# Performance work log

Hardware: AMD Instinct MI355X
Metric: run time of the kernel (lower is better)

## Reference

```python
import jax, jax.numpy as jnp
import numpy as np

E = 1024  # embed_dim
H = 16    # num_heads
D = E // H  # head_dim


def setup_inputs() -> dict:
    key = jax.random.key(0)
    ks = jax.random.split(key, 9)
    s = 0.02
    return {
        "hidden_state": jax.random.normal(ks[0], (4, 1024, E), jnp.float32),
        "Wq": jax.random.normal(ks[1], (H, D, E), jnp.float32) * s,
        "bq": jax.random.normal(ks[2], (H, D), jnp.float32) * s,
        "Wk": jax.random.normal(ks[3], (H, D, E), jnp.float32) * s,
        "bk": jax.random.normal(ks[4], (H, D), jnp.float32) * s,
        "Wv": jax.random.normal(ks[5], (H, D, E), jnp.float32) * s,
        "bv": jax.random.normal(ks[6], (H, D), jnp.float32) * s,
        "Wo": jax.random.normal(ks[7], (E, E), jnp.float32) * s,
        "bo": jax.random.normal(ks[8], (E,), jnp.float32) * s,
    }


def _mha(x, Wq, bq, Wk, bk, Wv, bv, Wo, bo):
    # Per-head linear projections (torch Linear: y = x W^T + b), batched over heads.
    q = jnp.einsum("bse,hde->bhsd", x, Wq) + bq[None, :, None, :]
    k = jnp.einsum("bse,hde->bhsd", x, Wk) + bk[None, :, None, :]
    v = jnp.einsum("bse,hde->bhsd", x, Wv) + bv[None, :, None, :]
    scores = jnp.einsum("bhsd,bhtd->bhst", q, k) / jnp.sqrt(jnp.asarray(D, x.dtype))
    w = jax.nn.softmax(scores, axis=-1)  # F.softmax default -> last dim
    o = jnp.einsum("bhst,bhtd->bhsd", w, v)
    # concat heads along last dim: [B,S,H*D] in head order (matches torch.cat)
    B, _, S, _ = o.shape
    o = jnp.transpose(o, (0, 2, 1, 3)).reshape(B, S, H * D)
    return o @ Wo.T + bo


def reference(hidden_state, Wq, bq, Wk, bk, Wv, bv, Wo, bo):
    return _mha(hidden_state, Wq, bq, Wk, bk, Wv, bv, Wo, bo)
```

## Files before the change

kernel.cpp:

```cpp
#include <hip/hip_runtime.h>
#include <hip/hip_bf16.h>
#include <stdint.h>

#define E_DIM 1024
#define H_NUM 16
#define D_DIM 64
#define B_NUM 4
#define S_LEN 1024

typedef __attribute__((ext_vector_type(8))) short bf16x8;
typedef __attribute__((ext_vector_type(4))) short bf16x4;
typedef __attribute__((ext_vector_type(4))) float f32x4;

__device__ inline ushort f2b(float x) {
    __hip_bfloat16 h = __float2bfloat16(x);
    return *(ushort*)&h;
}
__device__ inline uint pk2(float a, float b) {
    __hip_bfloat162 h = __float22bfloat162_rn(make_float2(a, b));
    return *(uint*)&h;
}

__device__ inline void gld16(const ushort* g, ushort* l) {
    __builtin_amdgcn_global_load_lds((const __attribute__((address_space(1))) void*)g,
                                     (__attribute__((address_space(3))) void*)l, 16, 0, 0);
}

__global__ __launch_bounds__(256)
void convert_all(const float* __restrict__ X,  const float* __restrict__ Wq,
                 const float* __restrict__ Wk, const float* __restrict__ Wv,
                 const float* __restrict__ Wo,
                 ushort* __restrict__ Xb, ushort* __restrict__ Wcat,
                 ushort* __restrict__ Wob)
{
    const int bid = blockIdx.x;
    const float* src; ushort* dst; size_t off;
    if (bid < 4096)      { src = X;  dst = Xb;   off = (size_t)bid * 1024; }
    else if (bid < 5120) { src = Wq; dst = Wcat;              off = (size_t)(bid - 4096) * 1024; }
    else if (bid < 6144) { src = Wk; dst = Wcat + (1u << 20); off = (size_t)(bid - 5120) * 1024; }
    else if (bid < 7168) { src = Wv; dst = Wcat + (2u << 20); off = (size_t)(bid - 6144) * 1024; }
    else                 { src = Wo; dst = Wob;               off = (size_t)(bid - 7168) * 1024; }
    const size_t i = off + (size_t)threadIdx.x * 4;
    float4 v = *(const float4*)&src[i];
    ushort4 o;
    o.x = f2b(v.x); o.y = f2b(v.y); o.z = f2b(v.z); o.w = f2b(v.w);
    *(ushort4*)&dst[i] = o;
}

template<int MODE>
__global__ __launch_bounds__(256)
void gemm128(const ushort* __restrict__ A, const ushort* __restrict__ Bw,
             const float* __restrict__ b0, const float* __restrict__ b1,
             const float* __restrict__ b2,
             ushort* __restrict__ Qb, ushort* __restrict__ Kb,
             ushort* __restrict__ Vt_g, float* __restrict__ Cout, int K)
{
    constexpr int BM = 128;
    constexpr int BN = (MODE == 0) ? 128 : 64;
    constexpr int MI = (MODE == 0) ? 4 : 2;
    constexpr int NI = 4;

    __shared__ ushort As[2][BM * 32];
    __shared__ ushort Bs[2][BN * 32];

    const int tid  = threadIdx.x;
    const int wave = tid >> 6;
    const int lane = tid & 63;
    const int quad = lane >> 4;
    const int l16  = lane & 15;
    const int wm   = (MODE == 0) ? (wave & 1) : wave;
    const int wn   = (MODE == 0) ? (wave >> 1) : 0;
    const int moff = wm * MI * 16;
    const int noff = wn * NI * 16;
    const int m0   = blockIdx.x * BM;
    const int n0   = blockIdx.y * BN;

    f32x4 acc[MI][NI] = {};

#pragma unroll
    for (int i = 0; i < BM / 64; ++i) {
        const int e = i * 256 + tid;
        gld16(&A[(size_t)(m0 + (e >> 2)) * K + (e & 3) * 8], &As[0][e * 8]);
    }
#pragma unroll
    for (int i = 0; i < BN / 64; ++i) {
        const int e = i * 256 + tid;
        gld16(&Bw[(size_t)(n0 + (e >> 2)) * K + (e & 3) * 8], &Bs[0][e * 8]);
    }
    __syncthreads();

    const int nk = K >> 5;
    for (int ki = 0; ki < nk; ++ki) {
        const int cur = ki & 1;
        if (ki + 1 < nk) {
            const int k0 = (ki + 1) << 5;
#pragma unroll
            for (int i = 0; i < BM / 64; ++i) {
                const int e = i * 256 + tid;
                gld16(&A[(size_t)(m0 + (e >> 2)) * K + k0 + (e & 3) * 8], &As[cur ^ 1][e * 8]);
            }
#pragma unroll
            for (int i = 0; i < BN / 64; ++i) {
                const int e = i * 256 + tid;
                gld16(&Bw[(size_t)(n0 + (e >> 2)) * K + k0 + (e & 3) * 8], &Bs[cur ^ 1][e * 8]);
            }
        }

        bf16x8 af[MI], bf[NI];
#pragma unroll
        for (int mi = 0; mi < MI; ++mi)
            af[mi] = *(const bf16x8*)&As[cur][(moff + mi * 16 + l16) * 32 + quad * 8];
#pragma unroll
        for (int ni = 0; ni < NI; ++ni)
            bf[ni] = *(const bf16x8*)&Bs[cur][(noff + ni * 16 + l16) * 32 + quad * 8];
#pragma unroll
        for (int mi = 0; mi < MI; ++mi)
#pragma unroll
            for (int ni = 0; ni < NI; ++ni)
                acc[mi][ni] = __builtin_amdgcn_mfma_f32_16x16x32_bf16(af[mi], bf[ni], acc[mi][ni], 0, 0, 0);
        __syncthreads();
    }

    if (MODE == 0) {
        const int seg = n0 >> 10;
        const float* bp = (seg == 0) ? b0 : (seg == 1) ? b1 : b2;
        if (seg < 2) {
            ushort* dst = (seg == 0) ? Qb : Kb;
#pragma unroll
            for (int ni = 0; ni < NI; ++ni) {
                const int c = (n0 + noff + ni * 16 + l16) & 1023;
                const float bv = bp[c];
#pragma unroll
                for (int mi = 0; mi < MI; ++mi)
#pragma unroll
                    for (int r = 0; r < 4; ++r) {
                        const int m = m0 + moff + mi * 16 + quad * 4 + r;
                        dst[(size_t)m * 1024 + c] = f2b(acc[mi][ni][r] + bv);
                    }
            }
        } else {
#pragma unroll
            for (int ni = 0; ni < NI; ++ni) {
                const int c  = (n0 + noff + ni * 16 + l16) & 1023;
                const int hh = c >> 6, d = c & 63;
                const float bv = bp[c];
#pragma unroll
                for (int mi = 0; mi < MI; ++mi) {
                    const int mb = m0 + moff + mi * 16 + quad * 4;
                    const int b  = mb >> 10, s = mb & 1023;
                    ushort4 pk;
                    pk.x = f2b(acc[mi][ni][0] + bv);
                    pk.y = f2b(acc[mi][ni][1] + bv);
                    pk.z = f2b(acc[mi][ni][2] + bv);
                    pk.w = f2b(acc[mi][ni][3] + bv);
                    *(ushort4*)&Vt_g[(((size_t)(b * 16 + hh)) * 64 + d) * 1024 + s] = pk;
                }
            }
        }
    } else {
#pragma unroll
        for (int ni = 0; ni < NI; ++ni) {
            const int n = n0 + noff + ni * 16 + l16;
            const float bv = b0[n];
#pragma unroll
            for (int mi = 0; mi < MI; ++mi)
#pragma unroll
                for (int r = 0; r < 4; ++r) {
                    const int m = m0 + moff + mi * 16 + quad * 4 + r;
                    Cout[(size_t)m * 1024 + n] = acc[mi][ni][r] + bv;
                }
        }
    }
}

__global__ __launch_bounds__(256)
void attention4(const ushort* __restrict__ Qg, const ushort* __restrict__ Kg,
                const ushort* __restrict__ Vg, ushort* __restrict__ Og)
{
    __shared__ ushort S[4][64][68];

    const int tid  = threadIdx.x;
    const int w    = tid >> 6;
    const int lane = tid & 63;
    const int quad = lane >> 4;
    const int l16  = lane & 15;

    const int qt = blockIdx.x;
    const int bh = blockIdx.y;
    const int b  = bh >> 4;
    const int h  = bh & 15;
    const size_t tbase = ((size_t)b * S_LEN) * E_DIM + (size_t)h * D_DIM;
    const size_t vbase = (size_t)bh * D_DIM * S_LEN;

    const int sr = tid >> 3;
    const int c8 = (tid & 7) * 8;

#pragma unroll
    for (int g = 0; g < 2; ++g) {
        const int rr = sr + g * 32;
        *(uint4*)&S[2][rr][c8] = *(const uint4*)&Qg[tbase + (size_t)(qt * 64 + rr) * E_DIM + c8];
        *(uint4*)&S[0][rr][c8] = *(const uint4*)&Kg[tbase + (size_t)rr * E_DIM + c8];
        *(uint4*)&S[1][rr][c8] = *(const uint4*)&Vg[vbase + (size_t)rr * S_LEN + c8];
    }
    __syncthreads();

    bf16x8 qf[2];
    qf[0] = *(const bf16x8*)&S[2][w * 16 + l16][quad * 8];
    qf[1] = *(const bf16x8*)&S[2][w * 16 + l16][32 + quad * 8];
    __syncthreads();

    float lq = 0.0f;
    f32x4 oacc[4] = {};
    const float C2 = 0.18033688011f;

    for (int kt = 0; kt < 16; ++kt) {
        const int cur = kt & 1;

        uint4 kpre[2], vpre[2];
        if (kt < 15) {
#pragma unroll
            for (int g = 0; g < 2; ++g) {
                const int rr = sr + g * 32;
                kpre[g] = *(const uint4*)&Kg[tbase + (size_t)((kt + 1) * 64 + rr) * E_DIM + c8];
                vpre[g] = *(const uint4*)&Vg[vbase + (size_t)rr * S_LEN + (kt + 1) * 64 + c8];
            }
        }

        f32x4 sacc[4] = {};
#pragma unroll
        for (int mt = 0; mt < 4; ++mt)
#pragma unroll
            for (int ks = 0; ks < 2; ++ks) {
                bf16x8 kf = *(const bf16x8*)&S[cur * 2][mt * 16 + l16][ks * 32 + quad * 8];
                sacc[mt] = __builtin_amdgcn_mfma_f32_16x16x32_bf16(kf, qf[ks], sacc[mt], 0, 0, 0);
            }

        float p[4][4], rs = 0.0f;
#pragma unroll
        for (int mt = 0; mt < 4; ++mt)
#pragma unroll
            for (int r = 0; r < 4; ++r) {
                p[mt][r] = exp2f(sacc[mt][r] * C2);
                rs += p[mt][r];
            }
        lq += rs;

        bf16x4 pf[4];
#pragma unroll
        for (int kb = 0; kb < 4; ++kb) {
            union { uint u[2]; bf16x4 v; } pk;
            pk.u[0] = pk2(p[kb][0], p[kb][1]);
            pk.u[1] = pk2(p[kb][2], p[kb][3]);
            pf[kb] = pk.v;
        }

#pragma unroll
        for (int nb = 0; nb < 4; ++nb)
#pragma unroll
            for (int kb = 0; kb < 4; ++kb) {
                bf16x4 vf = *(const bf16x4*)&S[cur * 2 + 1][nb * 16 + l16][kb * 16 + quad * 4];
                oacc[nb] = __builtin_amdgcn_mfma_f32_16x16x16bf16_1k(pf[kb], vf, oacc[nb], 0, 0, 0);
            }

        if (kt < 15) {
            const int nxt = cur ^ 1;
#pragma unroll
            for (int g = 0; g < 2; ++g) {
                const int rr = sr + g * 32;
                *(uint4*)&S[nxt * 2][rr][c8]     = kpre[g];
                *(uint4*)&S[nxt * 2 + 1][rr][c8] = vpre[g];
            }
        }
        __syncthreads();
    }

    lq += __shfl_xor(lq, 16);
    lq += __shfl_xor(lq, 32);
    const float linv = 1.0f / lq;
    float lC[4];
#pragma unroll
    for (int r = 0; r < 4; ++r) lC[r] = __shfl(linv, quad * 4 + r);
#pragma unroll
    for (int nb = 0; nb < 4; ++nb)
#pragma unroll
        for (int r = 0; r < 4; ++r) {
            const int q = qt * 64 + w * 16 + quad * 4 + r;
            const int d = nb * 16 + l16;
            Og[tbase + (size_t)q * E_DIM + d] = f2b(oacc[nb][r] * lC[r]);
        }
}

extern "C" void kernel_launch(void* const* d_in, const int* in_sizes, int n_in,
                              void* d_out, int out_size, void* d_ws, size_t ws_size,
                              hipStream_t stream)
{
    (void)in_sizes; (void)n_in; (void)out_size; (void)ws_size;

    const float* X  = (const float*)d_in[0];
    const float* Wq = (const float*)d_in[1];
    const float* bq = (const float*)d_in[2];
    const float* Wk = (const float*)d_in[3];
    const float* bk = (const float*)d_in[4];
    const float* Wv = (const float*)d_in[5];
    const float* bv = (const float*)d_in[6];
    const float* Wo = (const float*)d_in[7];
    const float* bo = (const float*)d_in[8];

    const size_t MEG = 1u << 20;
    ushort* ws   = (ushort*)d_ws;
    ushort* Xb   = ws;
    ushort* Wcat = ws + 4 * MEG;
    ushort* Wob  = ws + 7 * MEG;
    ushort* Qb   = ws + 8 * MEG;
    ushort* Kb   = ws + 12 * MEG;
    ushort* Vtg  = ws + 16 * MEG;
    ushort* AO   = Xb;

    dim3 blk(256);

    convert_all<<<8192, blk, 0, stream>>>(X, Wq, Wk, Wv, Wo, Xb, Wcat, Wob);

    gemm128<0><<<dim3(32, 24), blk, 0, stream>>>(Xb, Wcat, bq, bk, bv,
                                                 Qb, Kb, Vtg, nullptr, E_DIM);

    attention4<<<dim3(16, 64), blk, 0, stream>>>(Qb, Kb, Vtg, AO);

    gemm128<1><<<dim3(32, 16), blk, 0, stream>>>(AO, Wob, bo, nullptr, nullptr,
                                                 nullptr, nullptr, nullptr,
                                                 (float*)d_out, E_DIM);
}
```

Before: 203.0 us.

## Retile GEMMs, stage epilogues through LDS, fold softmax scale into Q, double attention rows

The QKV projection GEMM now uses 128x64 tiles, which doubles the grid. Its epilogue stages results through shared memory so that the row-major Q/K and the transposed V can be written with wide coalesced 16-byte stores; the output GEMM stages fp32 results the same way. The softmax scale (log2e/sqrt(D)) is folded into Q at projection time, so the attention kernel no longer multiplies scores before exp2. Each attention block now handles 128 query rows and reuses every K/V tile across two query groups, which halves K/V reloads at the cost of more registers and half as many blocks.

```diff
diff --git a/kernel.cpp b/kernel.cpp
--- a/kernel.cpp
+++ b/kernel.cpp
@@ -11,6 +11,8 @@
 typedef __attribute__((ext_vector_type(8))) short bf16x8;
 typedef __attribute__((ext_vector_type(4))) short bf16x4;
 typedef __attribute__((ext_vector_type(4))) float f32x4;
+
+#define SOFTMAX_C2 0.18033688011112042f
 
 __device__ inline ushort f2b(float x) {
     __hip_bfloat16 h = __float2bfloat16(x);
@@ -55,38 +57,28 @@
              ushort* __restrict__ Qb, ushort* __restrict__ Kb,
              ushort* __restrict__ Vt_g, float* __restrict__ Cout, int K)
 {
-    constexpr int BM = 128;
-    constexpr int BN = (MODE == 0) ? 128 : 64;
-    constexpr int MI = (MODE == 0) ? 4 : 2;
-    constexpr int NI = 4;
-
-    __shared__ ushort As[2][BM * 32];
-    __shared__ ushort Bs[2][BN * 32];
+    __shared__ __align__(16) ushort SM[12288];
+    ushort* As = SM;
+    ushort* Bs = SM + 8192;
 
     const int tid  = threadIdx.x;
     const int wave = tid >> 6;
     const int lane = tid & 63;
     const int quad = lane >> 4;
     const int l16  = lane & 15;
-    const int wm   = (MODE == 0) ? (wave & 1) : wave;
-    const int wn   = (MODE == 0) ? (wave >> 1) : 0;
-    const int moff = wm * MI * 16;
-    const int noff = wn * NI * 16;
-    const int m0   = blockIdx.x * BM;
-    const int n0   = blockIdx.y * BN;
-
-    f32x4 acc[MI][NI] = {};
-
-#pragma unroll
-    for (int i = 0; i < BM / 64; ++i) {
+    const int wm   = wave & 1;
+    const int wn   = wave >> 1;
+    const int m0   = blockIdx.x * 128;
+    const int n0   = blockIdx.y * 64;
+
+    f32x4 acc[4][2] = {};
+
+#pragma unroll
+    for (int i = 0; i < 2; ++i) {
         const int e = i * 256 + tid;
-        gld16(&A[(size_t)(m0 + (e >> 2)) * K + (e & 3) * 8], &As[0][e * 8]);
-    }
-#pragma unroll
-    for (int i = 0; i < BN / 64; ++i) {
-        const int e = i * 256 + tid;
-        gld16(&Bw[(size_t)(n0 + (e >> 2)) * K + (e & 3) * 8], &Bs[0][e * 8]);
-    }
+        gld16(&A[(size_t)(m0 + (e >> 2)) * K + (e & 3) * 8], &As[e * 8]);
+    }
+    gld16(&Bw[(size_t)(n0 + (tid >> 2)) * K + (tid & 3) * 8], &Bs[tid * 8]);
     __syncthreads();
 
     const int nk = K >> 5;
@@ -95,86 +87,117 @@
         if (ki + 1 < nk) {
             const int k0 = (ki + 1) << 5;
 #pragma unroll
-            for (int i = 0; i < BM / 64; ++i) {
+            for (int i = 0; i < 2; ++i) {
                 const int e = i * 256 + tid;
-                gld16(&A[(size_t)(m0 + (e >> 2)) * K + k0 + (e & 3) * 8], &As[cur ^ 1][e * 8]);
-            }
-#pragma unroll
-            for (int i = 0; i < BN / 64; ++i) {
-                const int e = i * 256 + tid;
-                gld16(&Bw[(size_t)(n0 + (e >> 2)) * K + k0 + (e & 3) * 8], &Bs[cur ^ 1][e * 8]);
-            }
-        }
-
-        bf16x8 af[MI], bf[NI];
-#pragma unroll
-        for (int mi = 0; mi < MI; ++mi)
-            af[mi] = *(const bf16x8*)&As[cur][(moff + mi * 16 + l16) * 32 + quad * 8];
-#pragma unroll
-        for (int ni = 0; ni < NI; ++ni)
-            bf[ni] = *(const bf16x8*)&Bs[cur][(noff + ni * 16 + l16) * 32 + quad * 8];
-#pragma unroll
-        for (int mi = 0; mi < MI; ++mi)
-#pragma unroll
-            for (int ni = 0; ni < NI; ++ni)
+                gld16(&A[(size_t)(m0 + (e >> 2)) * K + k0 + (e & 3) * 8],
+                      &As[(cur ^ 1) * 4096 + e * 8]);
+            }
+            gld16(&Bw[(size_t)(n0 + (tid >> 2)) * K + k0 + (tid & 3) * 8],
+                  &Bs[(cur ^ 1) * 2048 + tid * 8]);
+        }
+
+        bf16x8 af[4], bf[2];
+#pragma unroll
+        for (int mi = 0; mi < 4; ++mi)
+            af[mi] = *(const bf16x8*)&As[cur * 4096 + (wm * 64 + mi * 16 + l16) * 32 + quad * 8];
+#pragma unroll
+        for (int ni = 0; ni < 2; ++ni)
+            bf[ni] = *(const bf16x8*)&Bs[cur * 2048 + (wn * 32 + ni * 16 + l16) * 32 + quad * 8];
+#pragma unroll
+        for (int mi = 0; mi < 4; ++mi)
+#pragma unroll
+            for (int ni = 0; ni < 2; ++ni)
                 acc[mi][ni] = __builtin_amdgcn_mfma_f32_16x16x32_bf16(af[mi], bf[ni], acc[mi][ni], 0, 0, 0);
         __syncthreads();
     }
 
     if (MODE == 0) {
-        const int seg = n0 >> 10;
+        const int seg   = n0 >> 10;
+        const int cbase = n0 & 1023;
         const float* bp = (seg == 0) ? b0 : (seg == 1) ? b1 : b2;
+        const float scl = (seg == 0) ? SOFTMAX_C2 : 1.0f;
+
         if (seg < 2) {
+            ushort* T = SM;
+#pragma unroll
+            for (int ni = 0; ni < 2; ++ni) {
+                const int nloc = wn * 32 + ni * 16 + l16;
+                const float bv = bp[cbase + nloc];
+#pragma unroll
+                for (int mi = 0; mi < 4; ++mi)
+#pragma unroll
+                    for (int r = 0; r < 4; ++r)
+                        T[(wm * 64 + mi * 16 + quad * 4 + r) * 72 + nloc] =
+                            f2b((acc[mi][ni][r] + bv) * scl);
+            }
+            __syncthreads();
             ushort* dst = (seg == 0) ? Qb : Kb;
-#pragma unroll
-            for (int ni = 0; ni < NI; ++ni) {
-                const int c = (n0 + noff + ni * 16 + l16) & 1023;
-                const float bv = bp[c];
-#pragma unroll
-                for (int mi = 0; mi < MI; ++mi)
-#pragma unroll
-                    for (int r = 0; r < 4; ++r) {
-                        const int m = m0 + moff + mi * 16 + quad * 4 + r;
-                        dst[(size_t)m * 1024 + c] = f2b(acc[mi][ni][r] + bv);
-                    }
-            }
+            const int row = tid >> 1, half = tid & 1;
+            const ushort* s = &T[row * 72 + half * 32];
+            ushort* d = &dst[(size_t)(m0 + row) * 1024 + cbase + half * 32];
+#pragma unroll
+            for (int j = 0; j < 4; ++j)
+                *(uint4*)(d + j * 8) = *(const uint4*)(s + j * 8);
         } else {
-#pragma unroll
-            for (int ni = 0; ni < NI; ++ni) {
-                const int c  = (n0 + noff + ni * 16 + l16) & 1023;
-                const int hh = c >> 6, d = c & 63;
-                const float bv = bp[c];
-#pragma unroll
-                for (int mi = 0; mi < MI; ++mi) {
-                    const int mb = m0 + moff + mi * 16 + quad * 4;
-                    const int b  = mb >> 10, s = mb & 1023;
+            ushort* Tt = SM;
+            const int hh = cbase >> 6;
+            const int b  = m0 >> 10, sbase = m0 & 1023;
+#pragma unroll
+            for (int ni = 0; ni < 2; ++ni) {
+                const int nloc = wn * 32 + ni * 16 + l16;
+                const float bv = bp[cbase + nloc];
+#pragma unroll
+                for (int mi = 0; mi < 4; ++mi) {
+                    const int mloc = wm * 64 + mi * 16 + quad * 4;
                     ushort4 pk;
                     pk.x = f2b(acc[mi][ni][0] + bv);
                     pk.y = f2b(acc[mi][ni][1] + bv);
                     pk.z = f2b(acc[mi][ni][2] + bv);
                     pk.w = f2b(acc[mi][ni][3] + bv);
-                    *(ushort4*)&Vt_g[(((size_t)(b * 16 + hh)) * 64 + d) * 1024 + s] = pk;
+                    *(ushort4*)&Tt[nloc * 136 + mloc] = pk;
                 }
             }
+            __syncthreads();
+            const int nrow = tid >> 2, qtr = tid & 3;
+            const ushort* s = &Tt[nrow * 136 + qtr * 32];
+            ushort* d = &Vt_g[(((size_t)(b * 16 + hh)) * 64 + nrow) * 1024 + sbase + qtr * 32];
+#pragma unroll
+            for (int j = 0; j < 4; ++j)
+                *(uint4*)(d + j * 8) = *(const uint4*)(s + j * 8);
         }
     } else {
-#pragma unroll
-        for (int ni = 0; ni < NI; ++ni) {
-            const int n = n0 + noff + ni * 16 + l16;
-            const float bv = b0[n];
-#pragma unroll
-            for (int mi = 0; mi < MI; ++mi)
-#pragma unroll
-                for (int r = 0; r < 4; ++r) {
-                    const int m = m0 + moff + mi * 16 + quad * 4 + r;
-                    Cout[(size_t)m * 1024 + n] = acc[mi][ni][r] + bv;
+        float* Tf = (float*)SM;
+        float bv[2];
+#pragma unroll
+        for (int ni = 0; ni < 2; ++ni)
+            bv[ni] = b0[n0 + wn * 32 + ni * 16 + l16];
+#pragma unroll
+        for (int p = 0; p < 2; ++p) {
+            if (wm == p) {
+#pragma unroll
+                for (int ni = 0; ni < 2; ++ni) {
+                    const int nloc = wn * 32 + ni * 16 + l16;
+#pragma unroll
+                    for (int mi = 0; mi < 4; ++mi)
+#pragma unroll
+                        for (int r = 0; r < 4; ++r)
+                            Tf[(mi * 16 + quad * 4 + r) * 68 + nloc] = acc[mi][ni][r] + bv[ni];
                 }
+            }
+            __syncthreads();
+            const int row = tid >> 2, q4 = tid & 3;
+            const float* s = &Tf[row * 68 + q4 * 16];
+            float* d = &Cout[(size_t)(m0 + p * 64 + row) * 1024 + n0 + q4 * 16];
+#pragma unroll
+            for (int j = 0; j < 4; ++j)
+                *(float4*)(d + j * 4) = *(const float4*)(s + j * 4);
+            __syncthreads();
         }
     }
 }
 
 __global__ __launch_bounds__(256)
-void attention4(const ushort* __restrict__ Qg, const ushort* __restrict__ Kg,
+void attention5(const ushort* __restrict__ Qg, const ushort* __restrict__ Kg,
                 const ushort* __restrict__ Vg, ushort* __restrict__ Og)
 {
     __shared__ ushort S[4][64][68];
@@ -196,22 +219,29 @@
     const int c8 = (tid & 7) * 8;
 
 #pragma unroll
+    for (int g = 0; g < 4; ++g) {
+        const int rr = sr + g * 32;
+        *(uint4*)&S[2 + (rr >> 6)][rr & 63][c8] =
+            *(const uint4*)&Qg[tbase + (size_t)(qt * 128 + rr) * E_DIM + c8];
+    }
+#pragma unroll
     for (int g = 0; g < 2; ++g) {
         const int rr = sr + g * 32;
-        *(uint4*)&S[2][rr][c8] = *(const uint4*)&Qg[tbase + (size_t)(qt * 64 + rr) * E_DIM + c8];
         *(uint4*)&S[0][rr][c8] = *(const uint4*)&Kg[tbase + (size_t)rr * E_DIM + c8];
         *(uint4*)&S[1][rr][c8] = *(const uint4*)&Vg[vbase + (size_t)rr * S_LEN + c8];
     }
     __syncthreads();
 
-    bf16x8 qf[2];
-    qf[0] = *(const bf16x8*)&S[2][w * 16 + l16][quad * 8];
-    qf[1] = *(const bf16x8*)&S[2][w * 16 + l16][32 + quad * 8];
+    bf16x8 qf[2][2];
+#pragma unroll
+    for (int u = 0; u < 2; ++u) {
+        qf[u][0] = *(const bf16x8*)&S[2 + u][w * 16 + l16][quad * 8];
+        qf[u][1] = *(const bf16x8*)&S[2 + u][w * 16 + l16][32 + quad * 8];
+    }
     __syncthreads();
 
-    float lq = 0.0f;
-    f32x4 oacc[4] = {};
-    const float C2 = 0.18033688011f;
+    float lq[2] = {0.0f, 0.0f};
+    f32x4 oacc[2][4] = {};
 
     for (int kt = 0; kt < 16; ++kt) {
         const int cur = kt & 1;
@@ -226,32 +256,33 @@
             }
         }
 
-        f32x4 sacc[4] = {};
+        f32x4 sacc[2][4] = {};
 #pragma unroll
         for (int mt = 0; mt < 4; ++mt)
 #pragma unroll
             for (int ks = 0; ks < 2; ++ks) {
                 bf16x8 kf = *(const bf16x8*)&S[cur * 2][mt * 16 + l16][ks * 32 + quad * 8];
-                sacc[mt] = __builtin_amdgcn_mfma_f32_16x16x32_bf16(kf, qf[ks], sacc[mt], 0, 0, 0);
-            }
-
-        float p[4][4], rs = 0.0f;
-#pragma unroll
-        for (int mt = 0; mt < 4; ++mt)
-#pragma unroll
-            for (int r = 0; r < 4; ++r) {
-                p[mt][r] = exp2f(sacc[mt][r] * C2);
-                rs += p[mt][r];
-            }
-        lq += rs;
-
-        bf16x4 pf[4];
-#pragma unroll
-        for (int kb = 0; kb < 4; ++kb) {
-            union { uint u[2]; bf16x4 v; } pk;
-            pk.u[0] = pk2(p[kb][0], p[kb][1]);
-            pk.u[1] = pk2(p[kb][2], p[kb][3]);
-            pf[kb] = pk.v;
+                sacc[0][mt] = __builtin_amdgcn_mfma_f32_16x16x32_bf16(kf, qf[0][ks], sacc[0][mt], 0, 0, 0);
+                sacc[1][mt] = __builtin_amdgcn_mfma_f32_16x16x32_bf16(kf, qf[1][ks], sacc[1][mt], 0, 0, 0);
+            }
+
+        bf16x4 pf[2][4];
+#pragma unroll
+        for (int u = 0; u < 2; ++u) {
+            float rs = 0.0f;
+#pragma unroll
+            for (int mt = 0; mt < 4; ++mt) {
+                float p0 = exp2f(sacc[u][mt][0]);
+                float p1 = exp2f(sacc[u][mt][1]);
+                float p2 = exp2f(sacc[u][mt][2]);
+                float p3 = exp2f(sacc[u][mt][3]);
+                rs += (p0 + p1) + (p2 + p3);
+                union { uint uu[2]; bf16x4 v; } pk;
+                pk.uu[0] = pk2(p0, p1);
+                pk.uu[1] = pk2(p2, p3);
+                pf[u][mt] = pk.v;
+            }
+            lq[u] += rs;
         }
 
 #pragma unroll
@@ -259,7 +290,8 @@
 #pragma unroll
             for (int kb = 0; kb < 4; ++kb) {
                 bf16x4 vf = *(const bf16x4*)&S[cur * 2 + 1][nb * 16 + l16][kb * 16 + quad * 4];
-                oacc[nb] = __builtin_amdgcn_mfma_f32_16x16x16bf16_1k(pf[kb], vf, oacc[nb], 0, 0, 0);
+                oacc[0][nb] = __builtin_amdgcn_mfma_f32_16x16x16bf16_1k(pf[0][kb], vf, oacc[0][nb], 0, 0, 0);
+                oacc[1][nb] = __builtin_amdgcn_mfma_f32_16x16x16bf16_1k(pf[1][kb], vf, oacc[1][nb], 0, 0, 0);
             }
 
         if (kt < 15) {
@@ -274,20 +306,24 @@
         __syncthreads();
     }
 
-    lq += __shfl_xor(lq, 16);
-    lq += __shfl_xor(lq, 32);
-    const float linv = 1.0f / lq;
-    float lC[4];
-#pragma unroll
-    for (int r = 0; r < 4; ++r) lC[r] = __shfl(linv, quad * 4 + r);
-#pragma unroll
-    for (int nb = 0; nb < 4; ++nb)
-#pragma unroll
-        for (int r = 0; r < 4; ++r) {
-            const int q = qt * 64 + w * 16 + quad * 4 + r;
-            const int d = nb * 16 + l16;
-            Og[tbase + (size_t)q * E_DIM + d] = f2b(oacc[nb][r] * lC[r]);
-        }
+#pragma unroll
+    for (int u = 0; u < 2; ++u) {
+        float l = lq[u];
+        l += __shfl_xor(l, 16);
+        l += __shfl_xor(l, 32);
+        const float linv = 1.0f / l;
+        float lC[4];
+#pragma unroll
+        for (int r = 0; r < 4; ++r) lC[r] = __shfl(linv, quad * 4 + r);
+#pragma unroll
+        for (int nb = 0; nb < 4; ++nb)
+#pragma unroll
+            for (int r = 0; r < 4; ++r) {
+                const int q = qt * 128 + u * 64 + w * 16 + quad * 4 + r;
+                const int d = nb * 16 + l16;
+                Og[tbase + (size_t)q * E_DIM + d] = f2b(oacc[u][nb][r] * lC[r]);
+            }
+    }
 }
 
 extern "C" void kernel_launch(void* const* d_in, const int* in_sizes, int n_in,
@@ -320,10 +356,10 @@
 
     convert_all<<<8192, blk, 0, stream>>>(X, Wq, Wk, Wv, Wo, Xb, Wcat, Wob);
 
-    gemm128<0><<<dim3(32, 24), blk, 0, stream>>>(Xb, Wcat, bq, bk, bv,
+    gemm128<0><<<dim3(32, 48), blk, 0, stream>>>(Xb, Wcat, bq, bk, bv,
                                                  Qb, Kb, Vtg, nullptr, E_DIM);
 
-    attention4<<<dim3(16, 64), blk, 0, stream>>>(Qb, Kb, Vtg, AO);
+    attention5<<<dim3(8, 64), blk, 0, stream>>>(Qb, Kb, Vtg, AO);
 
     gemm128<1><<<dim3(32, 16), blk, 0, stream>>>(AO, Wob, bo, nullptr, nullptr,
                                                  nullptr, nullptr, nullptr,
```

Measured after the change: 208.1 us. 1.03x slower.
